# Performance work log

Hardware: AMD Instinct MI355X
Metric: run time of the kernel (lower is better)

## Reference

```python
import jax, jax.numpy as jnp
import numpy as np

B, C, E = 8192, 128, 64  # batch, n_cols, embedding_size


def setup_inputs() -> dict:
    key = jax.random.key(0)
    ks = jax.random.split(key, 10)
    s = lambda k, shape, scale=0.1: jax.random.normal(k, shape, jnp.float32) * scale
    return {
        "samples": jax.random.normal(ks[0], (B, C), jnp.float32),
        "W1": s(ks[1], (C, E)),        # per-column Linear(1,E) weight (squeezed)
        "b1": s(ks[2], (C, E)),
        "W2": s(ks[3], (C, E, E)),     # per-column Linear(E,E) weight [out,in]
        "b2": s(ks[4], (C, E)),
        "q": s(ks[5], (C, C), 1.0),    # per-column Embedding(1,C) weights stacked
        "P1": s(ks[6], (C, E, E)),     # per-column projection Linear(E,E)
        "pb1": s(ks[7], (C, E)),
        "P2": s(ks[8], (C, E)),        # per-column Linear(E,1) weight (squeezed)
        "pb2": s(ks[9], (C,)),
    }


def reference(samples, W1, b1, W2, b2, q, P1, pb1, P2, pb2):
    # Per-column value MLPs: Linear(1,E) -> ReLU -> Linear(E,E)
    h = jax.nn.relu(samples[:, :, None] * W1[None] + b1[None])          # [B,C,E]
    v = jnp.einsum('bce,cfe->bcf', h, W2) + b2[None]                    # [B,C,E]
    # L2 normalize along embedding dim (torch F.normalize eps=1e-12)
    v = v / jnp.maximum(jnp.linalg.norm(v, axis=2, keepdims=True), 1e-12)
    # Attention weights: softmax over each q row, then zero the diagonal
    w = jax.nn.softmax(q, axis=1) * (1.0 - jnp.eye(C, dtype=q.dtype))   # [C,C]
    ctx = jnp.einsum('cn,bne->bce', w, v)                               # [B,C,E]
    # Per-column target projection: Linear(E,E) -> ReLU -> Linear(E,1)
    h2 = jax.nn.relu(jnp.einsum('bce,cfe->bcf', ctx, P1) + pb1[None])   # [B,C,E]
    out = jnp.einsum('bce,ce->bc', h2, P2) + pb2[None]                  # [B,C]
    return out
```

## Files before the change

kernel.cpp:

```cpp
#include <hip/hip_runtime.h>
#include <hip/hip_bf16.h>
#include <cstdint>

#define C_DIM 128
#define E_DIM 64
#define B_DIM 8192

typedef __attribute__((ext_vector_type(8))) short short8;
typedef __attribute__((ext_vector_type(4))) float f32x4;

union Frag8 { short8 v; short s[8]; uint32_t u[4]; };

__device__ __forceinline__ unsigned short bfbits(float x) {
    union { __hip_bfloat16 h; unsigned short u; } cv;
    cv.h = __float2bfloat16(x);
    return cv.u;
}
__device__ __forceinline__ float bits2f(unsigned short b) {
    return __uint_as_float(((uint32_t)b) << 16);
}

__global__ __launch_bounds__(128) void k0_softmax(const float* __restrict__ q,
                                                  unsigned short* __restrict__ whi,
                                                  unsigned short* __restrict__ wlo) {
    const int c = blockIdx.x;
    const int t = threadIdx.x;
    __shared__ float redM[2], redS[2];
    float v = q[c * C_DIM + t];
    float m = v;
    #pragma unroll
    for (int o = 32; o > 0; o >>= 1) m = fmaxf(m, __shfl_xor(m, o));
    if ((t & 63) == 0) redM[t >> 6] = m;
    __syncthreads();
    m = fmaxf(redM[0], redM[1]);
    float e = expf(v - m);
    float s = e;
    #pragma unroll
    for (int o = 32; o > 0; o >>= 1) s += __shfl_xor(s, o);
    if ((t & 63) == 0) redS[t >> 6] = s;
    __syncthreads();
    s = redS[0] + redS[1];
    float w = e / s;
    if (t == c) w = 0.f;
    unsigned short hb = bfbits(w);
    whi[c * C_DIM + t] = hb;
    wlo[c * C_DIM + t] = bfbits(w - bits2f(hb));
}

__global__ __launch_bounds__(256) void kP_split(const float* __restrict__ src,
                                                unsigned short* __restrict__ hi,
                                                unsigned short* __restrict__ lo) {
    const int i = blockIdx.x * 256 + threadIdx.x;
    const float4 v = ((const float4*)src)[i];
    float f[4] = {v.x, v.y, v.z, v.w};
    unsigned short h[4], l[4];
    #pragma unroll
    for (int j = 0; j < 4; ++j) {
        h[j] = bfbits(f[j]);
        l[j] = bfbits(f[j] - bits2f(h[j]));
    }
    ((ushort4*)hi)[i] = make_ushort4(h[0], h[1], h[2], h[3]);
    ((ushort4*)lo)[i] = make_ushort4(l[0], l[1], l[2], l[3]);
}

__global__ __launch_bounds__(512, 4) void k1_value(
        const float* __restrict__ samples, const float* __restrict__ W1,
        const float* __restrict__ b1, const unsigned short* __restrict__ W2hi,
        const float* __restrict__ b2,
        uint32_t* __restrict__ vbuf, int rowOff) {
    __shared__ char sOut[32 * 1024];
    const int t = threadIdx.x;
    const int rt = blockIdx.x, cg = blockIdx.y;
    const int r0 = rt * 64;
    const int cl = t >> 6;
    const int lane = t & 63;
    const int lm = lane & 15, lg = lane >> 4;
    const int c = cg * 8 + cl;
    const uint32_t xb = (((uint32_t)lane & 8u) >> 1) | ((((uint32_t)lane >> 5) & 1u) << 3);

    float sv[4];
    #pragma unroll
    for (int mt = 0; mt < 4; ++mt)
        sv[mt] = samples[(size_t)(rowOff + r0 + mt * 16 + lm) * C_DIM + c];

    float b2r[4];
    #pragma unroll
    for (int nt = 0; nt < 4; ++nt) b2r[nt] = b2[(size_t)c * 64 + nt * 16 + lm];

    f32x4 acc[4][4];
    #pragma unroll
    for (int mt = 0; mt < 4; ++mt)
        #pragma unroll
        for (int nt = 0; nt < 4; ++nt)
            acc[mt][nt] = (f32x4){0.f, 0.f, 0.f, 0.f};

    #pragma unroll
    for (int ks = 0; ks < 2; ++ks) {
        const size_t wbase = ((size_t)c * 64) * 64 + ks * 32 + lg * 8;

        short8 bhA = *(const short8*)(W2hi + wbase + (size_t)(0 * 16 + lm) * 64);
        short8 bhB = *(const short8*)(W2hi + wbase + (size_t)(1 * 16 + lm) * 64);

        const float4 w1a = *(const float4*)(W1 + (size_t)c * 64 + ks * 32 + lg * 8);
        const float4 w1b = *(const float4*)(W1 + (size_t)c * 64 + ks * 32 + lg * 8 + 4);
        const float4 b1a = *(const float4*)(b1 + (size_t)c * 64 + ks * 32 + lg * 8);
        const float4 b1b = *(const float4*)(b1 + (size_t)c * 64 + ks * 32 + lg * 8 + 4);
        const float w1r[8] = {w1a.x, w1a.y, w1a.z, w1a.w, w1b.x, w1b.y, w1b.z, w1b.w};
        const float b1r[8] = {b1a.x, b1a.y, b1a.z, b1a.w, b1b.x, b1b.y, b1b.z, b1b.w};

        short8 afr[4];
        #pragma unroll
        for (int mt = 0; mt < 4; ++mt) {
            Frag8 af;
            #pragma unroll
            for (int j = 0; j < 8; ++j)
                af.s[j] = (short)bfbits(fmaxf(fmaf(sv[mt], w1r[j], b1r[j]), 0.f));
            afr[mt] = af.v;
        }

        {
            #pragma unroll
            for (int mt = 0; mt < 4; ++mt)
                acc[mt][0] = __builtin_amdgcn_mfma_f32_16x16x32_bf16(afr[mt], bhA, acc[mt][0], 0, 0, 0);
            bhA = *(const short8*)(W2hi + wbase + (size_t)(2 * 16 + lm) * 64);

            #pragma unroll
            for (int mt = 0; mt < 4; ++mt)
                acc[mt][1] = __builtin_amdgcn_mfma_f32_16x16x32_bf16(afr[mt], bhB, acc[mt][1], 0, 0, 0);
            bhB = *(const short8*)(W2hi + wbase + (size_t)(3 * 16 + lm) * 64);

            #pragma unroll
            for (int mt = 0; mt < 4; ++mt)
                acc[mt][2] = __builtin_amdgcn_mfma_f32_16x16x32_bf16(afr[mt], bhA, acc[mt][2], 0, 0, 0);

            #pragma unroll
            for (int mt = 0; mt < 4; ++mt)
                acc[mt][3] = __builtin_amdgcn_mfma_f32_16x16x32_bf16(afr[mt], bhB, acc[mt][3], 0, 0, 0);
        }
    }

    float rsc[4][4];
    #pragma unroll
    for (int mt = 0; mt < 4; ++mt)
        #pragma unroll
        for (int i = 0; i < 4; ++i) {
            float s2 = 0.f;
            #pragma unroll
            for (int nt = 0; nt < 4; ++nt) {
                float vv = acc[mt][nt][i] + b2r[nt];
                acc[mt][nt][i] = vv;
                s2 = fmaf(vv, vv, s2);
            }
            s2 += __shfl_xor(s2, 1); s2 += __shfl_xor(s2, 2);
            s2 += __shfl_xor(s2, 4); s2 += __shfl_xor(s2, 8);
            rsc[mt][i] = 1.f / fmaxf(sqrtf(s2), 1e-12f);
        }

    #pragma unroll
    for (int p = 0; p < 2; ++p) {
        if (p) __syncthreads();
        #pragma unroll
        for (int mh = 0; mh < 2; ++mh) {
            const int mt = p * 2 + mh;
            #pragma unroll
            for (int i = 0; i < 4; ++i) {
                const int rl = mh * 16 + lg * 4 + i;
                const uint32_t rowbase = (uint32_t)rl * 1024u;
                const uint32_t swz = (uint32_t)(rl & 7) << 4;
                #pragma unroll
                for (int nt = 0; nt < 4; ++nt) {
                    const int f = nt * 16 + lm;
                    const uint32_t bo = (rowbase + (uint32_t)f * 16u + (uint32_t)cl * 2u) ^ swz ^ xb;
                    *(unsigned short*)(sOut + bo) = bfbits(acc[mt][nt][i] * rsc[mt][i]);
                }
            }
        }
        __syncthreads();
        #pragma unroll
        for (int it = 0; it < 4; ++it) {
            const int unit = t + it * 512;
            const int rl = unit >> 6, f = unit & 63;
            const uint32_t lb = ((uint32_t)rl * 1024u + (uint32_t)f * 16u) ^ ((uint32_t)(rl & 7) << 4);
            uint4 val = *(const uint4*)(sOut + lb);
            if (it & 1) val = make_uint4(val.z, val.w, val.x, val.y);
            {
                const bool s0 = (t & 8) != 0;
                const uint32_t a = s0 ? val.y : val.x;
                const uint32_t b = s0 ? val.x : val.y;
                const uint32_t cc2 = s0 ? val.w : val.z;
                const uint32_t d = s0 ? val.z : val.w;
                val = make_uint4(a, b, cc2, d);
            }
            ((uint4*)vbuf)[((size_t)(r0 + p * 32 + rl) * 16 + cg) * 64 + f] = val;
        }
    }
}

__global__ __launch_bounds__(512) void k2_ctx(
        const unsigned short* __restrict__ whi,
        const uint32_t* __restrict__ vbuf, uint32_t* __restrict__ cbuf) {
    __shared__ char sC[65536];
    const int t = threadIdx.x;
    const int lane = t & 63, wv = t >> 6;
    const int lm = lane & 15, lg = lane >> 4;
    const int rloc = wv >> 1, ch = wv & 1;
    const size_t rbase = (size_t)blockIdx.x * 4;
    const size_t r = rbase + rloc;
    const char* vrow = (const char*)vbuf + (r << 14);

#define LDA(KS, ET) (*(const short8*)(vrow + ((KS) * 4 + lg) * 1024 + ((ET) * 16 + lm) * 16))
#define LDW(KS, NT) (*(const short8*)(whi + (size_t)(ch * 64 + (NT) * 16 + lm) * C_DIM + (KS) * 32 + lg * 8))

    f32x4 acc[4][4];
    #pragma unroll
    for (int et = 0; et < 4; ++et)
        #pragma unroll
        for (int nt = 0; nt < 4; ++nt)
            acc[et][nt] = (f32x4){0.f, 0.f, 0.f, 0.f};

    short8 afX[4], afY[4], w0[4];
    #pragma unroll
    for (int et = 0; et < 4; ++et) afX[et] = LDA(0, et);
    #pragma unroll
    for (int et = 0; et < 4; ++et) afY[et] = LDA(1, et);
    #pragma unroll
    for (int nt = 0; nt < 4; ++nt) w0[nt] = LDW(0, nt);

#define K2_MFMA(AF)                                                                        \
    _Pragma("unroll")                                                                      \
    for (int nt = 0; nt < 4; ++nt)                                                         \
        _Pragma("unroll")                                                                  \
        for (int et = 0; et < 4; ++et)                                                     \
            acc[et][nt] = __builtin_amdgcn_mfma_f32_16x16x32_bf16(AF[et], w0[nt],          \
                                                                  acc[et][nt], 0, 0, 0);
    K2_MFMA(afX)
    #pragma unroll
    for (int et = 0; et < 4; ++et) afX[et] = LDA(2, et);
    #pragma unroll
    for (int nt = 0; nt < 4; ++nt) w0[nt] = LDW(1, nt);
    K2_MFMA(afY)
    #pragma unroll
    for (int et = 0; et < 4; ++et) afY[et] = LDA(3, et);
    #pragma unroll
    for (int nt = 0; nt < 4; ++nt) w0[nt] = LDW(2, nt);
    K2_MFMA(afX)
    #pragma unroll
    for (int nt = 0; nt < 4; ++nt) w0[nt] = LDW(3, nt);
    K2_MFMA(afY)
#undef K2_MFMA
#undef LDA
#undef LDW

    char* srow = sC + rloc * 16384;
    #pragma unroll
    for (int et = 0; et < 4; ++et)
        #pragma unroll
        for (int nt = 0; nt < 4; ++nt) {
            const int cloc = ch * 64 + nt * 16 + lm;
            const uint32_t u0 = (uint32_t)bfbits(acc[et][nt][0]) | ((uint32_t)bfbits(acc[et][nt][1]) << 16);
            const uint32_t u1 = (uint32_t)bfbits(acc[et][nt][2]) | ((uint32_t)bfbits(acc[et][nt][3]) << 16);
            uint32_t bo = (uint32_t)cloc * 128u + (uint32_t)(et * 16 + lg * 4) * 2u;
            bo ^= (uint32_t)(cloc & 7) << 4;
            *(uint2*)(srow + bo) = make_uint2(u0, u1);
        }
    __syncthreads();

    #pragma unroll
    for (int it = 0; it < 8; ++it) {
        const int unit = t + it * 512;
        const int row = unit >> 10;
        const int u = unit & 1023;
        const uint32_t lb = (uint32_t)row * 16384u +
                            (((uint32_t)u * 16u) ^ ((((uint32_t)u >> 3) & 7u) << 4));
        const uint4 val = *(const uint4*)(sC + lb);
        ((uint4*)cbuf)[((rbase + row) << 10) + u] = val;
    }
}

__global__ __launch_bounds__(512) void k3_out(
        const uint32_t* __restrict__ cbuf, const unsigned short* __restrict__ P1hi,
        const unsigned short* __restrict__ P1lo, const float* __restrict__ pb1,
        const float* __restrict__ P2, const float* __restrict__ pb2,
        float* __restrict__ out, int rowOff) {
    __shared__ char sC[32 * 1024];
    const int t = threadIdx.x;
    const int cg = blockIdx.x;
    const int r0 = blockIdx.y * 32;
    const int lane = t & 63, wv = t >> 6;
    const int lm = lane & 15, lg = lane >> 4;
    const int cl = wv;
    const int c = cg * 8 + cl;

    {
        const int rr = t >> 6;
        const int inner = t & 63;
        #pragma unroll
        for (int p = 0; p < 4; ++p) {
            const int r = p * 8 + rr;
            const uint4 val = *(const uint4*)((const char*)cbuf +
                (size_t)(r0 + r) * 16384 + (size_t)cg * 1024 + (size_t)inner * 16);
            const uint32_t bo = ((uint32_t)r * 1024u + (uint32_t)inner * 16u) ^ ((uint32_t)(r & 7) << 4);
            *(uint4*)(sC + bo) = val;
        }
    }
    __syncthreads();

    float pb1r[4], p2r[4];
    #pragma unroll
    for (int nt = 0; nt < 4; ++nt) {
        pb1r[nt] = pb1[(size_t)c * 64 + nt * 16 + lm];
        p2r[nt]  = P2[(size_t)c * 64 + nt * 16 + lm];
    }
    const float pb2c = pb2[c];

    f32x4 acc[2][4];
    #pragma unroll
    for (int mt = 0; mt < 2; ++mt)
        #pragma unroll
        for (int nt = 0; nt < 4; ++nt)
            acc[mt][nt] = (f32x4){0.f, 0.f, 0.f, 0.f};

    #pragma unroll
    for (int ks = 0; ks < 2; ++ks) {
        short8 a[2];
        #pragma unroll
        for (int mt = 0; mt < 2; ++mt) {
            const int rl = mt * 16 + lm;
            const uint32_t bo = ((uint32_t)rl * 1024u + (uint32_t)cl * 128u +
                                 (uint32_t)ks * 64u + (uint32_t)lg * 16u) ^ ((uint32_t)(rl & 7) << 4);
            a[mt] = *(const short8*)(sC + bo);
        }
        #pragma unroll
        for (int nt = 0; nt < 4; ++nt) {
            const size_t wb = ((size_t)c * 64 + nt * 16 + lm) * 64 + ks * 32 + lg * 8;
            const short8 bh = *(const short8*)(P1hi + wb);
            const short8 bl = *(const short8*)(P1lo + wb);
            #pragma unroll
            for (int mt = 0; mt < 2; ++mt) {
                acc[mt][nt] = __builtin_amdgcn_mfma_f32_16x16x32_bf16(a[mt], bh, acc[mt][nt], 0, 0, 0);
                acc[mt][nt] = __builtin_amdgcn_mfma_f32_16x16x32_bf16(a[mt], bl, acc[mt][nt], 0, 0, 0);
            }
        }
    }

    #pragma unroll
    for (int mt = 0; mt < 2; ++mt)
        #pragma unroll
        for (int i = 0; i < 4; ++i) {
            float p = 0.f;
            #pragma unroll
            for (int nt = 0; nt < 4; ++nt)
                p = fmaf(fmaxf(acc[mt][nt][i] + pb1r[nt], 0.f), p2r[nt], p);
            p += __shfl_xor(p, 1); p += __shfl_xor(p, 2);
            p += __shfl_xor(p, 4); p += __shfl_xor(p, 8);
            if (lm == 0)
                out[(size_t)(rowOff + r0 + mt * 16 + lg * 4 + i) * C_DIM + c] = p + pb2c;
        }
}

extern "C" void kernel_launch(void* const* d_in, const int* in_sizes, int n_in,
                              void* d_out, int out_size, void* d_ws, size_t ws_size,
                              hipStream_t stream) {
    const float* samples = (const float*)d_in[0];
    const float* W1  = (const float*)d_in[1];
    const float* b1  = (const float*)d_in[2];
    const float* W2  = (const float*)d_in[3];
    const float* b2  = (const float*)d_in[4];
    const float* q   = (const float*)d_in[5];
    const float* P1  = (const float*)d_in[6];
    const float* pb1 = (const float*)d_in[7];
    const float* P2  = (const float*)d_in[8];
    const float* pb2 = (const float*)d_in[9];
    float* out = (float*)d_out;

    char* ws = (char*)d_ws;
    unsigned short* whi  = (unsigned short*)ws;
    unsigned short* wlo  = (unsigned short*)(ws + 32768);
    unsigned short* W2hi = (unsigned short*)(ws + 65536);
    unsigned short* W2lo = (unsigned short*)(ws + 65536 + 1048576);
    unsigned short* P1hi = (unsigned short*)(ws + 65536 + 2097152);
    unsigned short* P1lo = (unsigned short*)(ws + 65536 + 3145728);
    const size_t head = 65536 + 4194304;

    size_t avail = (ws_size > head) ? ws_size - head : 0;
    long maxRows = (long)(avail / ((size_t)2 * C_DIM * E_DIM * 2));
    maxRows = (maxRows / 256) * 256;
    if (maxRows > B_DIM) maxRows = B_DIM;
    if (maxRows < 256) maxRows = 256;

    uint32_t* vbuf = (uint32_t*)(ws + head);
    uint32_t* cbuf = (uint32_t*)(ws + head + (size_t)maxRows * 16384);

    k0_softmax<<<dim3(C_DIM), dim3(C_DIM), 0, stream>>>(q, whi, wlo);
    kP_split<<<dim3(512), 256, 0, stream>>>(W2, W2hi, W2lo);
    kP_split<<<dim3(512), 256, 0, stream>>>(P1, P1hi, P1lo);

    for (int off = 0; off < B_DIM; off += (int)maxRows) {
        const int rows = (int)(((long)(B_DIM - off) < maxRows) ? (long)(B_DIM - off) : maxRows);
        k1_value<<<dim3(rows / 64, 16), 512, 0, stream>>>(samples, W1, b1, W2hi, b2, vbuf, off);
        k2_ctx<<<dim3(rows / 4), 512, 0, stream>>>(whi, vbuf, cbuf);
        k3_out<<<dim3(16, rows / 32), 512, 0, stream>>>(cbuf, P1hi, P1lo, pb1, P2, pb2, out, off);
    }
}
```

Measured before the change: 226.4 us.

## Store ctx in column-major row-tile layout so k3 loads MFMA fragments directly

k2 now writes the context buffer as [column][row-tile][16 rows][64 elems], so each k3 wave can load its 16x64 A fragment straight from global memory without LDS staging or a block barrier. k3 is regridded to one column per block with each wave owning a 16-row tile, and launch bounds request more resident blocks. The cost is k2's global stores becoming more scattered (128-byte chunks per row spread across columns), and k3 reloads each column's P1 weights in every wave.

```diff
diff --git a/kernel.cpp b/kernel.cpp
--- a/kernel.cpp
+++ b/kernel.cpp
@@ -198,7 +198,7 @@
 
 __global__ __launch_bounds__(512) void k2_ctx(
         const unsigned short* __restrict__ whi,
-        const uint32_t* __restrict__ vbuf, uint32_t* __restrict__ cbuf) {
+        const uint32_t* __restrict__ vbuf, uint32_t* __restrict__ cbuf, int nrt) {
     __shared__ char sC[65536];
     const int t = threadIdx.x;
     const int lane = t & 63, wv = t >> 6;
@@ -270,40 +270,30 @@
         const int unit = t + it * 512;
         const int row = unit >> 10;
         const int u = unit & 1023;
+        const int cc = u >> 3, ec = u & 7;
         const uint32_t lb = (uint32_t)row * 16384u +
-                            (((uint32_t)u * 16u) ^ ((((uint32_t)u >> 3) & 7u) << 4));
+                            (((uint32_t)u * 16u) ^ (((uint32_t)cc & 7u) << 4));
         const uint4 val = *(const uint4*)(sC + lb);
-        ((uint4*)cbuf)[((rbase + row) << 10) + u] = val;
-    }
-}
-
-__global__ __launch_bounds__(512) void k3_out(
+        const size_t grow = rbase + row;
+        ((uint4*)cbuf)[(((size_t)cc * nrt + (grow >> 4)) * 16 + (grow & 15)) * 8 + ec] = val;
+    }
+}
+
+__global__ __launch_bounds__(512, 4) void k3_out(
         const uint32_t* __restrict__ cbuf, const unsigned short* __restrict__ P1hi,
         const unsigned short* __restrict__ P1lo, const float* __restrict__ pb1,
         const float* __restrict__ P2, const float* __restrict__ pb2,
-        float* __restrict__ out, int rowOff) {
-    __shared__ char sC[32 * 1024];
+        float* __restrict__ out, int rowOff, int nrt) {
     const int t = threadIdx.x;
-    const int cg = blockIdx.x;
-    const int r0 = blockIdx.y * 32;
     const int lane = t & 63, wv = t >> 6;
     const int lm = lane & 15, lg = lane >> 4;
-    const int cl = wv;
-    const int c = cg * 8 + cl;
-
-    {
-        const int rr = t >> 6;
-        const int inner = t & 63;
-        #pragma unroll
-        for (int p = 0; p < 4; ++p) {
-            const int r = p * 8 + rr;
-            const uint4 val = *(const uint4*)((const char*)cbuf +
-                (size_t)(r0 + r) * 16384 + (size_t)cg * 1024 + (size_t)inner * 16);
-            const uint32_t bo = ((uint32_t)r * 1024u + (uint32_t)inner * 16u) ^ ((uint32_t)(r & 7) << 4);
-            *(uint4*)(sC + bo) = val;
-        }
-    }
-    __syncthreads();
+    const int c = blockIdx.x;
+    const int rtile = blockIdx.y * 8 + wv;
+
+    const char* abase = (const char*)cbuf +
+        (((size_t)c * nrt + rtile) * 16 + lm) * 128 + (size_t)lg * 16;
+    const short8 a0 = *(const short8*)(abase);
+    const short8 a1 = *(const short8*)(abase + 64);
 
     float pb1r[4], p2r[4];
     #pragma unroll
@@ -313,49 +303,35 @@
     }
     const float pb2c = pb2[c];
 
-    f32x4 acc[2][4];
-    #pragma unroll
-    for (int mt = 0; mt < 2; ++mt)
+    f32x4 acc[4];
+    #pragma unroll
+    for (int nt = 0; nt < 4; ++nt) acc[nt] = (f32x4){0.f, 0.f, 0.f, 0.f};
+
+    #pragma unroll
+    for (int nt = 0; nt < 4; ++nt) {
+        const size_t wb0 = ((size_t)c * 64 + nt * 16 + lm) * 64 + 0 * 32 + lg * 8;
+        const size_t wb1 = ((size_t)c * 64 + nt * 16 + lm) * 64 + 1 * 32 + lg * 8;
+        const short8 bh0 = *(const short8*)(P1hi + wb0);
+        const short8 bl0 = *(const short8*)(P1lo + wb0);
+        const short8 bh1 = *(const short8*)(P1hi + wb1);
+        const short8 bl1 = *(const short8*)(P1lo + wb1);
+        acc[nt] = __builtin_amdgcn_mfma_f32_16x16x32_bf16(a0, bh0, acc[nt], 0, 0, 0);
+        acc[nt] = __builtin_amdgcn_mfma_f32_16x16x32_bf16(a0, bl0, acc[nt], 0, 0, 0);
+        acc[nt] = __builtin_amdgcn_mfma_f32_16x16x32_bf16(a1, bh1, acc[nt], 0, 0, 0);
+        acc[nt] = __builtin_amdgcn_mfma_f32_16x16x32_bf16(a1, bl1, acc[nt], 0, 0, 0);
+    }
+
+    #pragma unroll
+    for (int i = 0; i < 4; ++i) {
+        float p = 0.f;
         #pragma unroll
         for (int nt = 0; nt < 4; ++nt)
-            acc[mt][nt] = (f32x4){0.f, 0.f, 0.f, 0.f};
-
-    #pragma unroll
-    for (int ks = 0; ks < 2; ++ks) {
-        short8 a[2];
-        #pragma unroll
-        for (int mt = 0; mt < 2; ++mt) {
-            const int rl = mt * 16 + lm;
-            const uint32_t bo = ((uint32_t)rl * 1024u + (uint32_t)cl * 128u +
-                                 (uint32_t)ks * 64u + (uint32_t)lg * 16u) ^ ((uint32_t)(rl & 7) << 4);
-            a[mt] = *(const short8*)(sC + bo);
-        }
-        #pragma unroll
-        for (int nt = 0; nt < 4; ++nt) {
-            const size_t wb = ((size_t)c * 64 + nt * 16 + lm) * 64 + ks * 32 + lg * 8;
-            const short8 bh = *(const short8*)(P1hi + wb);
-            const short8 bl = *(const short8*)(P1lo + wb);
-            #pragma unroll
-            for (int mt = 0; mt < 2; ++mt) {
-                acc[mt][nt] = __builtin_amdgcn_mfma_f32_16x16x32_bf16(a[mt], bh, acc[mt][nt], 0, 0, 0);
-                acc[mt][nt] = __builtin_amdgcn_mfma_f32_16x16x32_bf16(a[mt], bl, acc[mt][nt], 0, 0, 0);
-            }
-        }
-    }
-
-    #pragma unroll
-    for (int mt = 0; mt < 2; ++mt)
-        #pragma unroll
-        for (int i = 0; i < 4; ++i) {
-            float p = 0.f;
-            #pragma unroll
-            for (int nt = 0; nt < 4; ++nt)
-                p = fmaf(fmaxf(acc[mt][nt][i] + pb1r[nt], 0.f), p2r[nt], p);
-            p += __shfl_xor(p, 1); p += __shfl_xor(p, 2);
-            p += __shfl_xor(p, 4); p += __shfl_xor(p, 8);
-            if (lm == 0)
-                out[(size_t)(rowOff + r0 + mt * 16 + lg * 4 + i) * C_DIM + c] = p + pb2c;
-        }
+            p = fmaf(fmaxf(acc[nt][i] + pb1r[nt], 0.f), p2r[nt], p);
+        p += __shfl_xor(p, 1); p += __shfl_xor(p, 2);
+        p += __shfl_xor(p, 4); p += __shfl_xor(p, 8);
+        if (lm == 0)
+            out[(size_t)(rowOff + rtile * 16 + lg * 4 + i) * C_DIM + c] = p + pb2c;
+    }
 }
 
 extern "C" void kernel_launch(void* const* d_in, const int* in_sizes, int n_in,
@@ -397,8 +373,9 @@
 
     for (int off = 0; off < B_DIM; off += (int)maxRows) {
         const int rows = (int)(((long)(B_DIM - off) < maxRows) ? (long)(B_DIM - off) : maxRows);
+        const int nrt = rows / 16;
         k1_value<<<dim3(rows / 64, 16), 512, 0, stream>>>(samples, W1, b1, W2hi, b2, vbuf, off);
-        k2_ctx<<<dim3(rows / 4), 512, 0, stream>>>(whi, vbuf, cbuf);
-        k3_out<<<dim3(16, rows / 32), 512, 0, stream>>>(cbuf, P1hi, P1lo, pb1, P2, pb2, out, off);
-    }
-}
+        k2_ctx<<<dim3(rows / 4), 512, 0, stream>>>(whi, vbuf, cbuf, nrt);
+        k3_out<<<dim3(C_DIM, rows / 128), 512, 0, stream>>>(cbuf, P1hi, P1lo, pb1, P2, pb2, out, off, nrt);
+    }
+}
```

Result: slower. 285.3 us (+26.0%).
